# Performance work log

Measured on AMD Instinct MI355X. Metric: run time of the kernel, lower is better.

## Reference

```python
import jax, jax.numpy as jnp
import numpy as np

N = 100_000   # nodes
E = 1_600_000 # edges
F = 128       # num_node_features
H = 128       # hidden_channels
C = 10        # num_classes
G = 128       # graphs in batch


def setup_inputs() -> dict:
    key = jax.random.key(0)
    ks = jax.random.split(key, 12)
    x = jax.random.normal(ks[0], (N, F), jnp.float32)
    edge_index = jax.random.randint(ks[1], (2, E), 0, N, dtype=jnp.int32)
    batch = jnp.sort(jax.random.randint(ks[2], (N,), 0, G, dtype=jnp.int32))
    s = 1.0 / np.sqrt(H)
    W0 = jax.random.normal(ks[3], (F, H), jnp.float32) * s
    b0 = jnp.zeros((H,), jnp.float32)
    W1 = jax.random.normal(ks[4], (H, H), jnp.float32) * s
    b1 = jnp.zeros((H,), jnp.float32)
    W2 = jax.random.normal(ks[5], (H, H), jnp.float32) * s
    b2 = jnp.zeros((H,), jnp.float32)
    Wlin = jax.random.normal(ks[6], (H, C), jnp.float32) * s
    blin = jnp.zeros((C,), jnp.float32)
    return {"x": x, "edge_index": edge_index, "batch": batch,
            "W0": W0, "b0": b0, "W1": W1, "b1": b1, "W2": W2, "b2": b2,
            "Wlin": Wlin, "blin": blin}


def gcn_conv(x, W, b, src, dst):
    """PyG GCNConv: symmetric-normalized aggregation with self-loops."""
    xw = x @ W  # [N, H]
    # degree from destination column, +1 for self-loop (gcn_norm)
    deg = jax.ops.segment_sum(jnp.ones(src.shape[0], xw.dtype), dst,
                              num_segments=N) + 1.0
    dinv = jax.lax.rsqrt(deg)  # deg^{-1/2}
    # edge messages: xw[src] * deg_src^{-1/2} * deg_dst^{-1/2}
    msg = xw[src] * (dinv[src] * dinv[dst])[:, None]  # [E, H]
    agg = jax.ops.segment_sum(msg, dst, num_segments=N)
    # self-loop contribution: xw * deg^{-1}
    return agg + xw * (dinv * dinv)[:, None] + b


def reference(x, edge_index, batch, W0, b0, W1, b1, W2, b2, Wlin, blin):
    src, dst = edge_index[0], edge_index[1]
    h = jax.nn.relu(gcn_conv(x, W0, b0, src, dst))
    h = jax.nn.relu(gcn_conv(h, W1, b1, src, dst))
    h = jax.nn.relu(gcn_conv(h, W2, b2, src, dst))
    # global_mean_pool over graph ids
    cnt = jax.ops.segment_sum(jnp.ones(N, h.dtype), batch, num_segments=G)
    pooled = jax.ops.segment_sum(h, batch, num_segments=G) / jnp.maximum(cnt, 1.0)[:, None]
    # dropout is identity in eval mode
    return pooled @ Wlin + blin  # [G, C]
```

## Files before the change

kernel.cpp:

```cpp
#include <hip/hip_runtime.h>

typedef short short8 __attribute__((ext_vector_type(8)));
typedef float f32x4 __attribute__((ext_vector_type(4)));

#define HDIM 128
#define SCAN_NB 256
#define SCAN_TPB 256

__device__ __forceinline__ ushort f2bf(float f) {
  uint u = __float_as_uint(f);
  u += 0x7fffu + ((u >> 16) & 1u);
  return (ushort)(u >> 16);
}
__device__ __forceinline__ float bflo(uint v){ return __uint_as_float(v << 16); }
__device__ __forceinline__ float bfhi(uint v){ return __uint_as_float(v & 0xffff0000u); }

__global__ __launch_bounds__(256) void k_deg(const int* __restrict__ dst, int E, int* __restrict__ degc,
                                             ushort* __restrict__ rank) {
  for (int e = blockIdx.x*blockDim.x + threadIdx.x; e < E; e += gridDim.x*blockDim.x) {
    int r = atomicAdd(&degc[dst[e]], 1);
    rank[e] = (ushort)r;
  }
}

__global__ __launch_bounds__(SCAN_TPB) void k_scanA(const int* __restrict__ degc, int N,
                                                    int* __restrict__ blocksum, float* __restrict__ dinv) {
  int ipt = (N + SCAN_NB*SCAN_TPB - 1) / (SCAN_NB*SCAN_TPB);
  int chunk = ipt * SCAN_TPB;
  int start = blockIdx.x * chunk + threadIdx.x * ipt;
  int s = 0;
  #pragma unroll
  for (int k = 0; k < 4; ++k) {
    if (k < ipt) {
      int i = start + k;
      if (i < N) { int d = degc[i]; s += d; dinv[i] = rsqrtf((float)d + 1.0f); }
    }
  }
  __shared__ int red[SCAN_TPB];
  int t = threadIdx.x;
  red[t] = s; __syncthreads();
  for (int off = SCAN_TPB/2; off > 0; off >>= 1) {
    if (t < off) red[t] += red[t+off];
    __syncthreads();
  }
  if (t == 0) blocksum[blockIdx.x] = red[0];
}

__global__ __launch_bounds__(SCAN_NB) void k_scanB(const int* __restrict__ blocksum,
    int* __restrict__ blockoff, int* __restrict__ totalN,
    const int* __restrict__ batch, int N, int G, float* __restrict__ inv_cnt) {
  int t = threadIdx.x;
  if (blockIdx.x == 0) {
    __shared__ int sh[SCAN_NB];
    sh[t] = blocksum[t];
    __syncthreads();
    for (int off = 1; off < SCAN_NB; off <<= 1) {
      int v = (t >= off) ? sh[t-off] : 0;
      __syncthreads();
      sh[t] += v;
      __syncthreads();
    }
    blockoff[t] = (t == 0) ? 0 : sh[t-1];
    if (t == SCAN_NB-1) *totalN = sh[t];
  } else {
    __shared__ int bnd[SCAN_NB+1];
    if (t <= G) {
      int lo = 0, hi = N;
      while (lo < hi) { int mid = (lo + hi) >> 1; if (batch[mid] < t) lo = mid + 1; else hi = mid; }
      bnd[t] = lo;
    }
    __syncthreads();
    if (t < G) {
      int c = bnd[t+1] - bnd[t];
      inv_cnt[t] = 1.0f / (float)max(c, 1);
    }
  }
}

__global__ __launch_bounds__(SCAN_TPB) void k_scanC(const int* __restrict__ degc, int N,
    const int* __restrict__ blockoff, const int* __restrict__ totalN, int* __restrict__ row_ptr) {
  int ipt = (N + SCAN_NB*SCAN_TPB - 1) / (SCAN_NB*SCAN_TPB);
  int chunk = ipt * SCAN_TPB;
  int start = blockIdx.x * chunk + threadIdx.x * ipt;
  int t = threadIdx.x;
  int vals[4];
  int s = 0;
  #pragma unroll
  for (int k = 0; k < 4; ++k) {
    int v = 0;
    if (k < ipt) { int i = start + k; if (i < N) v = degc[i]; }
    vals[k] = v; s += v;
  }
  __shared__ int sh[SCAN_TPB];
  sh[t] = s; __syncthreads();
  for (int off = 1; off < SCAN_TPB; off <<= 1) {
    int v = (t >= off) ? sh[t-off] : 0;
    __syncthreads();
    sh[t] += v;
    __syncthreads();
  }
  int run = blockoff[blockIdx.x] + ((t == 0) ? 0 : sh[t-1]);
  #pragma unroll
  for (int k = 0; k < 4; ++k) {
    if (k < ipt) { int i = start + k; if (i < N) row_ptr[i] = run; }
    run += vals[k];
  }
  if (blockIdx.x == 0 && t == 0) row_ptr[N] = *totalN;
}

__global__ __launch_bounds__(256) void k_fill(const int* __restrict__ src, const int* __restrict__ dst, int E,
    const float* __restrict__ dinv, const int* __restrict__ row_ptr, const ushort* __restrict__ rank,
    int2* __restrict__ epack) {
  for (int e = blockIdx.x*blockDim.x + threadIdx.x; e < E; e += gridDim.x*blockDim.x) {
    int s = src[e], d = dst[e];
    int pos = row_ptr[d] + (int)rank[e];
    float cf = dinv[s] * dinv[d];
    epack[pos] = make_int2(s, __float_as_int(cf));
  }
}

template<int IN_F32>
__global__ __launch_bounds__(256,1) void k_gemm(const void* __restrict__ in_, const float* __restrict__ W,
    ushort* __restrict__ xw, int N) {
  int lane = threadIdx.x & 63;
  int wid  = (blockIdx.x * blockDim.x + threadIdx.x) >> 6;
  int nw   = (gridDim.x * blockDim.x) >> 6;
  int colB = lane & 15;
  int krow = (lane >> 4) * 8;

  short8 bfr[8][4];
  #pragma unroll
  for (int nt = 0; nt < 8; ++nt)
    #pragma unroll
    for (int kc = 0; kc < 4; ++kc) {
      short8 t;
      #pragma unroll
      for (int j = 0; j < 8; ++j)
        t[j] = (short)f2bf(W[(kc*32 + krow + j)*HDIM + nt*16 + colB]);
      bfr[nt][kc] = t;
    }

  int strips = (N + 15) >> 4;
  for (int s = wid; s < strips; s += nw) {
    int ra = s*16 + (lane & 15);
    bool va = ra < N;
    short8 a[4];
    if (IN_F32) {
      const float* xin = (const float*)in_;
      #pragma unroll
      for (int kc = 0; kc < 4; ++kc) {
        short8 t = {0,0,0,0,0,0,0,0};
        if (va) {
          const float* p = xin + (size_t)ra*HDIM + kc*32 + krow;
          float4 lo4 = *(const float4*)p;
          float4 hi4 = *(const float4*)(p+4);
          t[0]=(short)f2bf(lo4.x); t[1]=(short)f2bf(lo4.y); t[2]=(short)f2bf(lo4.z); t[3]=(short)f2bf(lo4.w);
          t[4]=(short)f2bf(hi4.x); t[5]=(short)f2bf(hi4.y); t[6]=(short)f2bf(hi4.z); t[7]=(short)f2bf(hi4.w);
        }
        a[kc] = t;
      }
    } else {
      const ushort* hin = (const ushort*)in_;
      #pragma unroll
      for (int kc = 0; kc < 4; ++kc) {
        short8 t = {0,0,0,0,0,0,0,0};
        if (va) t = *(const short8*)(hin + (size_t)ra*HDIM + kc*32 + krow);
        a[kc] = t;
      }
    }
    f32x4 acc[8];
    #pragma unroll
    for (int nt = 0; nt < 8; ++nt) { acc[nt][0]=0.f; acc[nt][1]=0.f; acc[nt][2]=0.f; acc[nt][3]=0.f; }
    #pragma unroll
    for (int nt = 0; nt < 8; ++nt)
      #pragma unroll
      for (int kc = 0; kc < 4; ++kc)
        acc[nt] = __builtin_amdgcn_mfma_f32_16x16x32_bf16(a[kc], bfr[nt][kc], acc[nt], 0, 0, 0);

    int r0 = s*16 + (lane>>4)*4;
    #pragma unroll
    for (int nt = 0; nt < 8; ++nt) {
      int c = nt*16 + (lane&15);
      #pragma unroll
      for (int rg = 0; rg < 4; ++rg) {
        int rr = r0 + rg;
        if (rr < N) xw[(size_t)rr*HDIM + c] = f2bf(acc[nt][rg]);
      }
    }
  }
}

__global__ __launch_bounds__(256) void k_agg(const uint* __restrict__ xwu, const int2* __restrict__ epack,
    const int* __restrict__ row_ptr, const float* __restrict__ dinv, const float* __restrict__ bias,
    uint* __restrict__ hu, int N) {
  int lane = threadIdx.x & 63;
  int n = blockIdx.x*4 + (threadIdx.x >> 6);
  if (n >= N) return;
  int e0 = row_ptr[n], e1 = row_ptr[n+1];
  float a0 = 0.f, a1 = 0.f;
  for (int base = e0; base < e1; base += 64) {
    int cnt = min(64, e1 - base);
    int2 myp = make_int2(0, 0);
    if (lane < cnt) myp = epack[base + lane];
    for (int j = 0; j < cnt; j += 16) {
      #pragma unroll
      for (int u = 0; u < 16; ++u) {
        int idx = j + u;
        int   sN = __shfl(myp.x, idx);
        float cf = __int_as_float(__shfl(myp.y, idx));
        uint v = xwu[(size_t)sN*64 + lane];
        a0 += cf * bflo(v);
        a1 += cf * bfhi(v);
      }
    }
  }
  float di = dinv[n]; float w = di*di;
  uint v = xwu[(size_t)n*64 + lane];
  a0 += w * bflo(v);
  a1 += w * bfhi(v);
  a0 += bias[lane*2];  a1 += bias[lane*2+1];
  a0 = fmaxf(a0, 0.f); a1 = fmaxf(a1, 0.f);
  uint o = ((uint)f2bf(a0)) | (((uint)f2bf(a1)) << 16);
  hu[(size_t)n*64 + lane] = o;
}

__global__ __launch_bounds__(256) void k_pool(const uint* __restrict__ hu, const int* __restrict__ batch,
    float* __restrict__ psum, int N) {
  int lane = threadIdx.x & 63;
  int wave = threadIdx.x >> 6;
  int n0 = blockIdx.x*512 + wave*128;
  if (n0 >= N) return;
  int n1 = min(n0 + 128, N);
  float a0 = 0.f, a1 = 0.f;
  int gc = batch[n0];
  for (int n = n0; n < n1; ++n) {
    int g = batch[n];
    if (g != gc) {
      atomicAdd(&psum[gc*HDIM + lane*2],   a0);
      atomicAdd(&psum[gc*HDIM + lane*2+1], a1);
      a0 = 0.f; a1 = 0.f; gc = g;
    }
    uint v = hu[(size_t)n*64 + lane];
    a0 += bflo(v); a1 += bfhi(v);
  }
  atomicAdd(&psum[gc*HDIM + lane*2],   a0);
  atomicAdd(&psum[gc*HDIM + lane*2+1], a1);
}

__global__ __launch_bounds__(256) void k_final(const float* __restrict__ psum, const float* __restrict__ inv_cnt,
    const float* __restrict__ Wlin, const float* __restrict__ blin, float* __restrict__ out, int G, int C) {
  int idx = blockIdx.x*256 + threadIdx.x;
  if (idx >= G*C) return;
  int g = idx / C, c = idx % C;
  float acc = 0.f;
  for (int k = 0; k < HDIM; ++k) acc += psum[g*HDIM + k] * Wlin[k*C + c];
  out[idx] = acc * inv_cnt[g] + blin[c];
}

extern "C" void kernel_launch(void* const* d_in, const int* in_sizes, int n_in,
                              void* d_out, int out_size, void* d_ws, size_t ws_size,
                              hipStream_t stream) {
  const float* x    = (const float*)d_in[0];
  const int*   ei   = (const int*)d_in[1];
  const int*   batch= (const int*)d_in[2];
  const float* W0   = (const float*)d_in[3];
  const float* b0   = (const float*)d_in[4];
  const float* W1   = (const float*)d_in[5];
  const float* b1   = (const float*)d_in[6];
  const float* W2   = (const float*)d_in[7];
  const float* b2   = (const float*)d_in[8];
  const float* Wlin = (const float*)d_in[9];
  const float* blin = (const float*)d_in[10];

  int N = in_sizes[0] / HDIM;
  int E = in_sizes[1] / 2;
  int C = in_sizes[10];
  int G = out_size / C;
  const int* src = ei;
  const int* dst = ei + E;

  char* ws = (char*)d_ws;
  size_t o = 0;
  auto alloc = [&](size_t bytes){ size_t r = o; o += (bytes + 511) & ~(size_t)511; return r; };
  size_t zbeg  = o;
  int*    degc    = (int*)   (ws + alloc((size_t)N*4));
  float*  psum    = (float*) (ws + alloc((size_t)G*HDIM*4));
  size_t zend  = o;
  float*  dinv    = (float*) (ws + alloc((size_t)N*4));
  int*    row_ptr = (int*)   (ws + alloc((size_t)(N+1)*4));
  float*  inv_cnt = (float*) (ws + alloc((size_t)G*4));
  int*    blocksum= (int*)   (ws + alloc((size_t)SCAN_NB*4));
  int*    blockoff= (int*)   (ws + alloc((size_t)SCAN_NB*4));
  int*    totalN  = (int*)   (ws + alloc(4));
  ushort* rank    = (ushort*)(ws + alloc((size_t)E*2));
  int2*   epack   = (int2*)  (ws + alloc((size_t)E*8));
  ushort* xw      = (ushort*)(ws + alloc((size_t)N*HDIM*2));
  ushort* hbuf    = (ushort*)(ws + alloc((size_t)N*HDIM*2));

  hipMemsetAsync(ws + zbeg, 0, zend - zbeg, stream);

  k_deg  <<<2048, 256, 0, stream>>>(dst, E, degc, rank);
  k_scanA<<<SCAN_NB, SCAN_TPB, 0, stream>>>(degc, N, blocksum, dinv);
  k_scanB<<<2, SCAN_NB, 0, stream>>>(blocksum, blockoff, totalN, batch, N, G, inv_cnt);
  k_scanC<<<SCAN_NB, SCAN_TPB, 0, stream>>>(degc, N, blockoff, totalN, row_ptr);
  k_fill <<<2048, 256, 0, stream>>>(src, dst, E, dinv, row_ptr, rank, epack);

  const int gemm_blocks = 512;
  const int agg_blocks  = (N + 3) / 4;

  k_gemm<1><<<gemm_blocks, 256, 0, stream>>>((const void*)x, W0, xw, N);
  k_agg<<<agg_blocks, 256, 0, stream>>>((const uint*)xw, epack, row_ptr, dinv, b0, (uint*)hbuf, N);
  k_gemm<0><<<gemm_blocks, 256, 0, stream>>>((const void*)hbuf, W1, xw, N);
  k_agg<<<agg_blocks, 256, 0, stream>>>((const uint*)xw, epack, row_ptr, dinv, b1, (uint*)hbuf, N);
  k_gemm<0><<<gemm_blocks, 256, 0, stream>>>((const void*)hbuf, W2, xw, N);
  k_agg<<<agg_blocks, 256, 0, stream>>>((const uint*)xw, epack, row_ptr, dinv, b2, (uint*)hbuf, N);

  k_pool<<<(N + 511)/512, 256, 0, stream>>>((const uint*)hbuf, batch, psum, N);
  k_final<<<(G*C + 255)/256, 256, 0, stream>>>(psum, inv_cnt, Wlin, blin, (float*)d_out, G, C);
}
```

Baseline: 407.7 us.

## Stage GEMM weights and output tiles through LDS for coalesced access

The GEMM kernel now loads W once per block with coalesced float4 reads, converts it to bf16 in shared memory, and has each wave pull its MFMA B fragments from there. Before, every wave did strided scalar global reads. Output tiles are also staged in shared memory so that each row is written as 16-byte vector stores instead of scattered 2-byte stores. The degree kernel switches from a grid-stride loop to one thread per edge. The block-wide barriers in the strip loop force waves to run in lockstep, and they add shared-memory traffic.

```diff
diff --git a/kernel.cpp b/kernel.cpp
--- a/kernel.cpp
+++ b/kernel.cpp
@@ -17,10 +17,8 @@
 
 __global__ __launch_bounds__(256) void k_deg(const int* __restrict__ dst, int E, int* __restrict__ degc,
                                              ushort* __restrict__ rank) {
-  for (int e = blockIdx.x*blockDim.x + threadIdx.x; e < E; e += gridDim.x*blockDim.x) {
-    int r = atomicAdd(&degc[dst[e]], 1);
-    rank[e] = (ushort)r;
-  }
+  int e = blockIdx.x*256 + threadIdx.x;
+  if (e < E) rank[e] = (ushort)atomicAdd(&degc[dst[e]], 1);
 }
 
 __global__ __launch_bounds__(SCAN_TPB) void k_scanA(const int* __restrict__ degc, int N,
@@ -122,28 +120,46 @@
 template<int IN_F32>
 __global__ __launch_bounds__(256,1) void k_gemm(const void* __restrict__ in_, const float* __restrict__ W,
     ushort* __restrict__ xw, int N) {
-  int lane = threadIdx.x & 63;
-  int wid  = (blockIdx.x * blockDim.x + threadIdx.x) >> 6;
-  int nw   = (gridDim.x * blockDim.x) >> 6;
+  __shared__ ushort wsh[8][4][64][8];
+  __shared__ ushort csh[4][16][136];
+
+  int tid  = threadIdx.x;
+  int lane = tid & 63;
+  int wave = tid >> 6;
+
+  #pragma unroll
+  for (int k = 0; k < 16; ++k) {
+    int idx4 = k*256 + tid;
+    float4 v = *(const float4*)(W + (size_t)idx4*4);
+    #pragma unroll
+    for (int m = 0; m < 4; ++m) {
+      int w = idx4*4 + m;
+      float f = (m==0) ? v.x : (m==1) ? v.y : (m==2) ? v.z : v.w;
+      int row = w >> 7, col = w & 127;
+      wsh[col>>4][row>>5][((row&31)>>3)*16 + (col&15)][row&7] = f2bf(f);
+    }
+  }
+  __syncthreads();
+
+  short8 bfr[8][4];
+  #pragma unroll
+  for (int nt = 0; nt < 8; ++nt)
+    #pragma unroll
+    for (int kc = 0; kc < 4; ++kc)
+      bfr[nt][kc] = *(const short8*)&wsh[nt][kc][lane][0];
+
   int colB = lane & 15;
   int krow = (lane >> 4) * 8;
-
-  short8 bfr[8][4];
-  #pragma unroll
-  for (int nt = 0; nt < 8; ++nt)
-    #pragma unroll
-    for (int kc = 0; kc < 4; ++kc) {
-      short8 t;
-      #pragma unroll
-      for (int j = 0; j < 8; ++j)
-        t[j] = (short)f2bf(W[(kc*32 + krow + j)*HDIM + nt*16 + colB]);
-      bfr[nt][kc] = t;
-    }
-
   int strips = (N + 15) >> 4;
-  for (int s = wid; s < strips; s += nw) {
-    int ra = s*16 + (lane & 15);
-    bool va = ra < N;
+  int nslots = gridDim.x * 4;
+  int slot   = blockIdx.x * 4 + wave;
+  int iters  = (strips + nslots - 1) / nslots;
+
+  for (int it = 0; it < iters; ++it) {
+    int s = it * nslots + slot;
+    bool vs = s < strips;
+    int ra = s*16 + colB;
+    bool va = vs && (ra < N);
     short8 a[4];
     if (IN_F32) {
       const float* xin = (const float*)in_;
@@ -177,16 +193,26 @@
       for (int kc = 0; kc < 4; ++kc)
         acc[nt] = __builtin_amdgcn_mfma_f32_16x16x32_bf16(a[kc], bfr[nt][kc], acc[nt], 0, 0, 0);
 
-    int r0 = s*16 + (lane>>4)*4;
-    #pragma unroll
-    for (int nt = 0; nt < 8; ++nt) {
-      int c = nt*16 + (lane&15);
-      #pragma unroll
-      for (int rg = 0; rg < 4; ++rg) {
-        int rr = r0 + rg;
-        if (rr < N) xw[(size_t)rr*HDIM + c] = f2bf(acc[nt][rg]);
+    if (vs) {
+      #pragma unroll
+      for (int nt = 0; nt < 8; ++nt)
+        #pragma unroll
+        for (int rg = 0; rg < 4; ++rg)
+          csh[wave][(lane>>4)*4 + rg][nt*16 + colB] = f2bf(acc[nt][rg]);
+    }
+    __syncthreads();
+    if (vs) {
+      #pragma unroll
+      for (int rb = 0; rb < 4; ++rb) {
+        int r  = rb*4 + (lane>>4);
+        int rr = s*16 + r;
+        if (rr < N) {
+          uint4 v = *(const uint4*)&csh[wave][r][(lane&15)*8];
+          *(uint4*)(xw + (size_t)rr*HDIM + (lane&15)*8) = v;
+        }
       }
     }
+    __syncthreads();
   }
 }
 
@@ -299,7 +325,7 @@
 
   hipMemsetAsync(ws + zbeg, 0, zend - zbeg, stream);
 
-  k_deg  <<<2048, 256, 0, stream>>>(dst, E, degc, rank);
+  k_deg  <<<(E+255)/256, 256, 0, stream>>>(dst, E, degc, rank);
   k_scanA<<<SCAN_NB, SCAN_TPB, 0, stream>>>(degc, N, blocksum, dinv);
   k_scanB<<<2, SCAN_NB, 0, stream>>>(blocksum, blockoff, totalN, batch, N, G, inv_cnt);
   k_scanC<<<SCAN_NB, SCAN_TPB, 0, stream>>>(degc, N, blockoff, totalN, row_ptr);
```

Measured after the change: 412.6 us. Within noise of the previous version (+1.2%).

## Privatize degree-count atomics per XCD to keep them in local L2

Applied to the files above, without the earlier changes.

The degree-count atomics are split into eight per-XCD planes, chosen by reading the XCC id hardware register. Each atomic uses workgroup scope, so it can resolve in that die's L2 instead of going device-wide. The scan kernels then sum the planes and build per-XCD row offsets, and the fill kernel places each edge using the XCD id packed into its rank. The costs are eight times the counter and offset memory, a larger memset, and extra reads in the scans. Correctness depends on workgroup-scope atomics being coherent across the CUs of one XCD and on per-plane in-degree staying below 8192.

```diff
diff --git a/kernel.cpp b/kernel.cpp
--- a/kernel.cpp
+++ b/kernel.cpp
@@ -6,6 +6,7 @@
 #define HDIM 128
 #define SCAN_NB 256
 #define SCAN_TPB 256
+#define XCC_GETREG_IMM (20 | (31 << 11))
 
 __device__ __forceinline__ ushort f2bf(float f) {
   uint u = __float_as_uint(f);
@@ -15,16 +16,19 @@
 __device__ __forceinline__ float bflo(uint v){ return __uint_as_float(v << 16); }
 __device__ __forceinline__ float bfhi(uint v){ return __uint_as_float(v & 0xffff0000u); }
 
-__global__ __launch_bounds__(256) void k_deg(const int* __restrict__ dst, int E, int* __restrict__ degc,
-                                             ushort* __restrict__ rank) {
+__global__ __launch_bounds__(256) void k_deg(const int* __restrict__ dst, int E, int N,
+                                             int* __restrict__ degc8, ushort* __restrict__ rank) {
+  uint xcd = __builtin_amdgcn_s_getreg(XCC_GETREG_IMM) & 7u;
+  int* plane = degc8 + (size_t)xcd * N;
   for (int e = blockIdx.x*blockDim.x + threadIdx.x; e < E; e += gridDim.x*blockDim.x) {
-    int r = atomicAdd(&degc[dst[e]], 1);
-    rank[e] = (ushort)r;
-  }
-}
-
-__global__ __launch_bounds__(SCAN_TPB) void k_scanA(const int* __restrict__ degc, int N,
-                                                    int* __restrict__ blocksum, float* __restrict__ dinv) {
+    int d = dst[e];
+    int r = __hip_atomic_fetch_add(&plane[d], 1, __ATOMIC_RELAXED, __HIP_MEMORY_SCOPE_WORKGROUP);
+    rank[e] = (ushort)((xcd << 13) | (uint)r);
+  }
+}
+
+__global__ __launch_bounds__(SCAN_TPB) void k_scanA(const int* __restrict__ degc8, int N,
+    int* __restrict__ degc, int* __restrict__ blocksum, float* __restrict__ dinv) {
   int ipt = (N + SCAN_NB*SCAN_TPB - 1) / (SCAN_NB*SCAN_TPB);
   int chunk = ipt * SCAN_TPB;
   int start = blockIdx.x * chunk + threadIdx.x * ipt;
@@ -33,7 +37,14 @@
   for (int k = 0; k < 4; ++k) {
     if (k < ipt) {
       int i = start + k;
-      if (i < N) { int d = degc[i]; s += d; dinv[i] = rsqrtf((float)d + 1.0f); }
+      if (i < N) {
+        int d = 0;
+        #pragma unroll
+        for (int x = 0; x < 8; ++x) d += degc8[(size_t)x*N + i];
+        degc[i] = d;
+        s += d;
+        dinv[i] = rsqrtf((float)d + 1.0f);
+      }
     }
   }
   __shared__ int red[SCAN_TPB];
@@ -77,8 +88,10 @@
   }
 }
 
-__global__ __launch_bounds__(SCAN_TPB) void k_scanC(const int* __restrict__ degc, int N,
-    const int* __restrict__ blockoff, const int* __restrict__ totalN, int* __restrict__ row_ptr) {
+__global__ __launch_bounds__(SCAN_TPB) void k_scanC(const int* __restrict__ degc,
+    const int* __restrict__ degc8, int N,
+    const int* __restrict__ blockoff, const int* __restrict__ totalN,
+    int* __restrict__ row_ptr, int* __restrict__ row_ptr8) {
   int ipt = (N + SCAN_NB*SCAN_TPB - 1) / (SCAN_NB*SCAN_TPB);
   int chunk = ipt * SCAN_TPB;
   int start = blockIdx.x * chunk + threadIdx.x * ipt;
@@ -102,18 +115,32 @@
   int run = blockoff[blockIdx.x] + ((t == 0) ? 0 : sh[t-1]);
   #pragma unroll
   for (int k = 0; k < 4; ++k) {
-    if (k < ipt) { int i = start + k; if (i < N) row_ptr[i] = run; }
+    if (k < ipt) {
+      int i = start + k;
+      if (i < N) {
+        row_ptr[i] = run;
+        int c = run;
+        #pragma unroll
+        for (int x = 0; x < 8; ++x) {
+          row_ptr8[(size_t)x*N + i] = c;
+          c += degc8[(size_t)x*N + i];
+        }
+      }
+    }
     run += vals[k];
   }
   if (blockIdx.x == 0 && t == 0) row_ptr[N] = *totalN;
 }
 
-__global__ __launch_bounds__(256) void k_fill(const int* __restrict__ src, const int* __restrict__ dst, int E,
-    const float* __restrict__ dinv, const int* __restrict__ row_ptr, const ushort* __restrict__ rank,
+__global__ __launch_bounds__(256) void k_fill(const int* __restrict__ src, const int* __restrict__ dst, int E, int N,
+    const float* __restrict__ dinv, const int* __restrict__ row_ptr8, const ushort* __restrict__ rank,
     int2* __restrict__ epack) {
   for (int e = blockIdx.x*blockDim.x + threadIdx.x; e < E; e += gridDim.x*blockDim.x) {
     int s = src[e], d = dst[e];
-    int pos = row_ptr[d] + (int)rank[e];
+    uint rk = rank[e];
+    uint xcd = rk >> 13;
+    int  r   = (int)(rk & 0x1FFFu);
+    int pos = row_ptr8[(size_t)xcd*N + d] + r;
     float cf = dinv[s] * dinv[d];
     epack[pos] = make_int2(s, __float_as_int(cf));
   }
@@ -283,11 +310,13 @@
   size_t o = 0;
   auto alloc = [&](size_t bytes){ size_t r = o; o += (bytes + 511) & ~(size_t)511; return r; };
   size_t zbeg  = o;
-  int*    degc    = (int*)   (ws + alloc((size_t)N*4));
+  int*    degc8   = (int*)   (ws + alloc((size_t)8*N*4));
   float*  psum    = (float*) (ws + alloc((size_t)G*HDIM*4));
   size_t zend  = o;
+  int*    degc    = (int*)   (ws + alloc((size_t)N*4));
   float*  dinv    = (float*) (ws + alloc((size_t)N*4));
   int*    row_ptr = (int*)   (ws + alloc((size_t)(N+1)*4));
+  int*    row_ptr8= (int*)   (ws + alloc((size_t)8*N*4));
   float*  inv_cnt = (float*) (ws + alloc((size_t)G*4));
   int*    blocksum= (int*)   (ws + alloc((size_t)SCAN_NB*4));
   int*    blockoff= (int*)   (ws + alloc((size_t)SCAN_NB*4));
@@ -299,11 +328,11 @@
 
   hipMemsetAsync(ws + zbeg, 0, zend - zbeg, stream);
 
-  k_deg  <<<2048, 256, 0, stream>>>(dst, E, degc, rank);
-  k_scanA<<<SCAN_NB, SCAN_TPB, 0, stream>>>(degc, N, blocksum, dinv);
+  k_deg  <<<2048, 256, 0, stream>>>(dst, E, N, degc8, rank);
+  k_scanA<<<SCAN_NB, SCAN_TPB, 0, stream>>>(degc8, N, degc, blocksum, dinv);
   k_scanB<<<2, SCAN_NB, 0, stream>>>(blocksum, blockoff, totalN, batch, N, G, inv_cnt);
-  k_scanC<<<SCAN_NB, SCAN_TPB, 0, stream>>>(degc, N, blockoff, totalN, row_ptr);
-  k_fill <<<2048, 256, 0, stream>>>(src, dst, E, dinv, row_ptr, rank, epack);
+  k_scanC<<<SCAN_NB, SCAN_TPB, 0, stream>>>(degc, degc8, N, blockoff, totalN, row_ptr, row_ptr8);
+  k_fill <<<2048, 256, 0, stream>>>(src, dst, E, N, dinv, row_ptr8, rank, epack);
 
   const int gemm_blocks = 512;
   const int agg_blocks  = (N + 3) / 4;
```

After: 404.8 us. About the same (-0.7%).
